# Performance work log

Hardware: AMD Instinct MI355X
Metric: run time of the kernel (lower is better)

## Reference

```python
import jax, jax.numpy as jnp
import numpy as np

V, E, P, T = 65536, 4096, 4096, 512
SENT = 1e9    # finite sentinel for masked min/max (keeps grads NaN-free)
BIG = 1e30    # 'never the minimum' sentinel for invalid points


def setup_inputs() -> dict:
    key = jax.random.key(0)
    k1, k2, k3, k4 = jax.random.split(key, 4)
    verts = jax.random.uniform(k1, (V, 3), dtype=jnp.float32)
    e0 = jax.random.randint(k2, (E,), 0, V - 1)
    edges = jnp.stack([e0, e0 + 1], axis=1)          # distinct endpoints
    listAll = jax.random.randint(k3, (P,), 0, V)
    TableR = jax.random.uniform(k4, (T, 7), dtype=jnp.float32)
    return {"verts": verts, "TableR": TableR, "edges": edges,
            "listAll": listAll, "epoch": 1, "pth": 0}


def _mouth_loss(verts, TableR, edges, listAll):
    v2 = verts[:, :2]                 # deleteaxeZ
    p = v2[listAll]                   # [P,2] query points
    px, py = p[:, 0], p[:, 1]
    ev = v2[edges]                    # [E,2,2]
    x0, y0 = ev[:, 0, 0], ev[:, 0, 1]
    x1, y1 = ev[:, 1, 0], ev[:, 1, 1]
    a = (y0 - y1) / (x0 - x1)         # edge line y = a*x + b (order-invariant)
    b = y0 - a * x0

    # getexpose: first edge with min_x < px < max_x (falls back to last edge)
    xmn, xmx = jnp.minimum(x0, x1), jnp.maximum(x0, x1)
    condA = (px[:, None] > xmn[None, :]) & (px[:, None] < xmx[None, :])  # [P,E]
    idx = jnp.where(condA.any(1), jnp.argmax(condA, axis=1), E - 1)
    exposeY = a[idx] * px + b[idx]
    L1 = jnp.sqrt((py - exposeY) ** 2)        # expose shares x with p -> dx=0
    cy = (py + exposeY) * 0.5                 # centre1 = midpoint (cx == px)
    cx = px

    # getpoints: intersections of horizontal ray y=cy with every edge
    ymn, ymx = jnp.minimum(y0, y1), jnp.maximum(y0, y1)
    condB = (cy[:, None] > ymn[None, :]) & (cy[:, None] < ymx[None, :])  # [P,E]
    xi = (cy[:, None] - b[None, :]) / a[None, :]                          # [P,E]
    n = condB.sum(1)
    xall_mx = jnp.max(jnp.where(condB, xi, -SENT), axis=1)
    xall_mn = jnp.min(jnp.where(condB, xi, SENT), axis=1)
    spu = condB & (xi >= cx[:, None])   # right side (incl. equal, per original)
    inf_ = condB & (xi < cx[:, None])   # left side
    xs = jnp.min(jnp.where(spu, xi, SENT), axis=1)    # minimum of spu
    xinf = jnp.max(jnp.where(inf_, xi, -SENT), axis=1)  # maximum of inf
    has_both = spu.any(1) & inf_.any(1)
    valid = (n == 2) | ((n > 2) & has_both)
    dx = jnp.where(n == 2, xall_mx - xall_mn, xs - xinf)
    L2 = jnp.sqrt(dx ** 2)                    # both points share y=cy
    d1 = jnp.sqrt((cy - 1.0) ** 2)            # dist([1, cy], Ref=(1,1))
    d2 = jnp.sqrt((px - 1.0) ** 2)            # dist([px, 1], Ref=(1,1))

    # al vs every table row (only columns 3..6 are used by the original)
    al = (jnp.abs(L1[:, None] - TableR[None, :, 3])
          + jnp.abs(L2[:, None] - TableR[None, :, 4])
          + jnp.abs(d1[:, None] - TableR[None, :, 5])
          + jnp.abs(d2[:, None] - TableR[None, :, 6]))          # [P,T]
    pm = jnp.min(al, axis=1)                  # per-point best table match
    # `error` is never reset in the original -> running min across points
    m = jnp.where(valid, pm, BIG)
    run = jax.lax.cummin(m, axis=0)
    return jnp.sum(jnp.where(valid, run, 0.0))


def reference(verts, TableR, edges, listAll, epoch, pth):
    # epoch/pth only gate .obj file dumping in the original; no math effect.
    return _mouth_loss(verts, TableR, edges, listAll)
```

## Files before the change

### kernel.cpp

```cpp
#include <hip/hip_runtime.h>
#include <math.h>

#define NV 65536
#define NE 4096
#define NP 4096
#define NT 512
#define SENTF 1000000000.0f
#define BIGF 1e30f

__device__ __forceinline__ float waveMinF(float v) {
    #pragma unroll
    for (int o = 32; o; o >>= 1) v = fminf(v, __shfl_xor(v, o, 64));
    return v;
}
__device__ __forceinline__ float waveMaxF(float v) {
    #pragma unroll
    for (int o = 32; o; o >>= 1) v = fmaxf(v, __shfl_xor(v, o, 64));
    return v;
}
__device__ __forceinline__ int waveSumI(int v) {
    #pragma unroll
    for (int o = 32; o; o >>= 1) v += __shfl_xor(v, o, 64);
    return v;
}
__device__ __forceinline__ int waveMinI(int v) {
    #pragma unroll
    for (int o = 32; o; o >>= 1) v = min(v, __shfl_xor(v, o, 64));
    return v;
}

__global__ void prep_kernel(const float* __restrict__ verts,
                            const int*   __restrict__ edges,
                            const float* __restrict__ tab,
                            float*  __restrict__ ea,  float*  __restrict__ eb,
                            float2* __restrict__ pk2, float4* __restrict__ pk4,
                            float4* __restrict__ tb4) {
    int e = blockIdx.x * blockDim.x + threadIdx.x;
    if (e < NT) {
        const float* r = tab + 7 * e;
        tb4[e] = make_float4(r[3], r[4], r[5], r[6]);
    }
    if (e >= NE) return;
    int i0 = edges[2 * e + 0];
    int i1 = edges[2 * e + 1];
    float x0 = verts[3 * i0 + 0], y0 = verts[3 * i0 + 1];
    float x1 = verts[3 * i1 + 0], y1 = verts[3 * i1 + 1];
    float a = (y0 - y1) / (x0 - x1);
    float b = y0 - a * x0;
    ea[e] = a; eb[e] = b;
    pk2[e] = make_float2(fminf(x0, x1), fmaxf(x0, x1));
    pk4[e] = make_float4(fminf(y0, y1), fmaxf(y0, y1), 1.0f / a, b);
}

__global__ __launch_bounds__(256) void point_kernel(
        const float*  __restrict__ verts,
        const int*    __restrict__ listAll,
        const float*  __restrict__ ea,  const float*  __restrict__ eb,
        const float2* __restrict__ pk2, const float4* __restrict__ pk4,
        const float4* __restrict__ tb4,
        float* __restrict__ mOut, int* __restrict__ validOut) {
    __shared__ int   sIdx[2][2];
    __shared__ float sMx[2][2], sMn[2][2], sXs[2][2], sXi[2][2];
    __shared__ int   sPk[2][2];
    __shared__ float sPm[2][2];

    int tid  = threadIdx.x;
    int lane = tid & 63;
    int wid  = tid >> 6;
    int pr   = wid >> 1;
    int half = wid & 1;
    int p    = blockIdx.x * 2 + pr;

    int   vi = listAll[p];
    float px = verts[3 * vi + 0];
    float py = verts[3 * vi + 1];

    const int base = half * (NE / 2);

    int minIdx = NE;
    for (int it = 0; it < (NE / 2) / 64; ++it) {
        int e = base + it * 64 + lane;
        float2 q = pk2[e];
        bool hit = (px > q.x) && (px < q.y);
        if (hit) minIdx = e;
        if (__any(hit)) break;
    }
    minIdx = waveMinI(minIdx);
    if (lane == 0) sIdx[pr][half] = minIdx;
    __syncthreads();
    int idx = min(sIdx[pr][0], sIdx[pr][1]);
    if (idx >= NE) idx = NE - 1;

    float exposeY = ea[idx] * px + eb[idx];
    float L1 = fabsf(py - exposeY);
    float cy = 0.5f * (py + exposeY);
    float cx = px;

    int   n = 0, hasS = 0, hasI = 0;
    float xallmx = -SENTF, xallmn = SENTF;
    float xs = SENTF, xinf = -SENTF;
    #pragma unroll 8
    for (int e = base + lane; e < base + (NE / 2); e += 64) {
        float4 q = pk4[e];
        bool  c  = (cy > q.x) && (cy < q.y);
        float xi = (cy - q.w) * q.z;
        n += c ? 1 : 0;
        xallmx = fmaxf(xallmx, c ? xi : -SENTF);
        xallmn = fminf(xallmn, c ? xi :  SENTF);
        bool sp = c && (xi >= cx);
        bool in_ = c && (xi <  cx);
        xs   = fminf(xs,   sp  ? xi :  SENTF);
        xinf = fmaxf(xinf, in_ ? xi : -SENTF);
        hasS |= sp ? 1 : 0;
        hasI |= in_ ? 1 : 0;
    }
    int packed = n | (hasS << 16) | (hasI << 24);
    packed = waveSumI(packed);
    xallmx = waveMaxF(xallmx);
    xallmn = waveMinF(xallmn);
    xs     = waveMinF(xs);
    xinf   = waveMaxF(xinf);
    if (lane == 0) {
        sPk[pr][half] = packed;
        sMx[pr][half] = xallmx; sMn[pr][half] = xallmn;
        sXs[pr][half] = xs;     sXi[pr][half] = xinf;
    }
    __syncthreads();
    {
        int pkA = sPk[pr][0], pkB = sPk[pr][1];
        n    = (pkA & 0xFFFF) + (pkB & 0xFFFF);
        hasS = ((pkA >> 16) & 0xFF) + ((pkB >> 16) & 0xFF);
        hasI = ((pkA >> 24) & 0xFF) + ((pkB >> 24) & 0xFF);
        xallmx = fmaxf(sMx[pr][0], sMx[pr][1]);
        xallmn = fminf(sMn[pr][0], sMn[pr][1]);
        xs     = fminf(sXs[pr][0], sXs[pr][1]);
        xinf   = fmaxf(sXi[pr][0], sXi[pr][1]);
    }

    bool valid = (n == 2) || ((n > 2) && (hasS > 0) && (hasI > 0));
    float dx = (n == 2) ? (xallmx - xallmn) : (xs - xinf);
    float L2 = fabsf(dx);
    float d1 = fabsf(cy - 1.0f);
    float d2 = fabsf(px - 1.0f);

    float pm = INFINITY;
    #pragma unroll
    for (int k = 0; k < 4; k++) {
        int t = half * (NT / 2) + k * 64 + lane;
        float4 r = tb4[t];
        float al = fabsf(L1 - r.x) + fabsf(L2 - r.y) +
                   fabsf(d1 - r.z) + fabsf(d2 - r.w);
        pm = fminf(pm, al);
    }
    pm = waveMinF(pm);
    if (lane == 0) sPm[pr][half] = pm;
    __syncthreads();

    if (half == 0 && lane == 0) {
        float pmin = fminf(sPm[pr][0], sPm[pr][1]);
        mOut[p]     = valid ? pmin : BIGF;
        validOut[p] = valid ? 1 : 0;
    }
}

__global__ __launch_bounds__(1024) void scan_kernel(const float* __restrict__ m,
                                                    const int*   __restrict__ valid,
                                                    float* __restrict__ out) {
    __shared__ float wAgg[16];
    __shared__ float wSum[16];
    int t = threadIdx.x;
    int lane = t & 63, wid = t >> 6;

    float v[4]; int vl[4];
    #pragma unroll
    for (int j = 0; j < 4; j++) { v[j] = m[4 * t + j]; vl[j] = valid[4 * t + j]; }
    float cmin = fminf(fminf(v[0], v[1]), fminf(v[2], v[3]));

    float inc = cmin;
    #pragma unroll
    for (int o = 1; o < 64; o <<= 1) {
        float u = __shfl_up(inc, o, 64);
        if (lane >= o) inc = fminf(inc, u);
    }
    if (lane == 63) wAgg[wid] = inc;
    __syncthreads();

    float wavePrefix = INFINITY;
    for (int i = 0; i < wid; i++) wavePrefix = fminf(wavePrefix, wAgg[i]);
    float excl = __shfl_up(inc, 1, 64);
    if (lane == 0) excl = INFINITY;
    float run = fminf(wavePrefix, excl);

    float sum = 0.0f;
    #pragma unroll
    for (int j = 0; j < 4; j++) {
        run = fminf(run, v[j]);
        if (vl[j]) sum += run;
    }
    #pragma unroll
    for (int o = 32; o; o >>= 1) sum += __shfl_xor(sum, o, 64);
    if (lane == 0) wSum[wid] = sum;
    __syncthreads();
    if (t == 0) {
        float s = 0.0f;
        for (int i = 0; i < 16; i++) s += wSum[i];
        out[0] = s;
    }
}

extern "C" void kernel_launch(void* const* d_in, const int* in_sizes, int n_in,
                              void* d_out, int out_size, void* d_ws, size_t ws_size,
                              hipStream_t stream) {
    const float* verts   = (const float*)d_in[0];
    const float* tab     = (const float*)d_in[1];
    const int*   edges   = (const int*)d_in[2];
    const int*   listAll = (const int*)d_in[3];

    char* ws = (char*)d_ws;
    float4* pk4 = (float4*)ws;                     ws += NE * sizeof(float4);
    float4* tb4 = (float4*)ws;                     ws += NT * sizeof(float4);
    float2* pk2 = (float2*)ws;                     ws += NE * sizeof(float2);
    float*  ea  = (float*)ws;                      ws += NE * sizeof(float);
    float*  eb  = (float*)ws;                      ws += NE * sizeof(float);
    float*  mArr= (float*)ws;                      ws += NP * sizeof(float);
    int*    vArr= (int*)ws;

    prep_kernel<<<(NE + 255) / 256, 256, 0, stream>>>(verts, edges, tab, ea, eb, pk2, pk4, tb4);
    point_kernel<<<NP / 2, 256, 0, stream>>>(verts, listAll, ea, eb, pk2, pk4, tb4, mArr, vArr);
    scan_kernel<<<1, 1024, 0, stream>>>(mArr, vArr, (float*)d_out);
}
```

Baseline: 27.42 us.

## Stage edge data in shared memory and assign one wave per point

Point blocks now have 1024 threads and handle 16 points, one wave each. Each block loads the whole packed edge array (64 KB) into LDS once, and every wave reuses it for the ray-intersection scan, which removes repeated global/L2 loads of the same data. Cross-wave shared-memory reductions and most barriers are dropped because each wave covers all edges and table rows for its point. In exchange the block uses 64 KB of LDS, which limits occupancy, and each wave runs a scan twice as long.

Result: slower. 28.94 us (+5.6%).

```diff
diff --git a/kernel.cpp b/kernel.cpp
--- a/kernel.cpp
+++ b/kernel.cpp
@@ -52,62 +52,63 @@
     pk4[e] = make_float4(fminf(y0, y1), fmaxf(y0, y1), 1.0f / a, b);
 }
 
-__global__ __launch_bounds__(256) void point_kernel(
+__global__ __launch_bounds__(1024) void point_kernel(
         const float*  __restrict__ verts,
         const int*    __restrict__ listAll,
         const float*  __restrict__ ea,  const float*  __restrict__ eb,
         const float2* __restrict__ pk2, const float4* __restrict__ pk4,
         const float4* __restrict__ tb4,
         float* __restrict__ mOut, int* __restrict__ validOut) {
-    __shared__ int   sIdx[2][2];
-    __shared__ float sMx[2][2], sMn[2][2], sXs[2][2], sXi[2][2];
-    __shared__ int   sPk[2][2];
-    __shared__ float sPm[2][2];
+    __shared__ float4 sE[NE];
 
     int tid  = threadIdx.x;
     int lane = tid & 63;
     int wid  = tid >> 6;
-    int pr   = wid >> 1;
-    int half = wid & 1;
-    int p    = blockIdx.x * 2 + pr;
+    int p    = blockIdx.x * 16 + wid;
+
+    float4 r0 = pk4[tid];
+    float4 r1 = pk4[1024 + tid];
+    float4 r2 = pk4[2048 + tid];
+    float4 r3 = pk4[3072 + tid];
 
     int   vi = listAll[p];
     float px = verts[3 * vi + 0];
     float py = verts[3 * vi + 1];
 
-    const int base = half * (NE / 2);
-
     int minIdx = NE;
-    for (int it = 0; it < (NE / 2) / 64; ++it) {
-        int e = base + it * 64 + lane;
+    for (int it = 0; it < NE / 64; ++it) {
+        int e = it * 64 + lane;
         float2 q = pk2[e];
         bool hit = (px > q.x) && (px < q.y);
         if (hit) minIdx = e;
         if (__any(hit)) break;
     }
     minIdx = waveMinI(minIdx);
-    if (lane == 0) sIdx[pr][half] = minIdx;
-    __syncthreads();
-    int idx = min(sIdx[pr][0], sIdx[pr][1]);
-    if (idx >= NE) idx = NE - 1;
+    int idx = (minIdx >= NE) ? (NE - 1) : minIdx;
 
     float exposeY = ea[idx] * px + eb[idx];
     float L1 = fabsf(py - exposeY);
     float cy = 0.5f * (py + exposeY);
     float cx = px;
 
+    sE[tid]        = r0;
+    sE[1024 + tid] = r1;
+    sE[2048 + tid] = r2;
+    sE[3072 + tid] = r3;
+    __syncthreads();
+
     int   n = 0, hasS = 0, hasI = 0;
     float xallmx = -SENTF, xallmn = SENTF;
     float xs = SENTF, xinf = -SENTF;
     #pragma unroll 8
-    for (int e = base + lane; e < base + (NE / 2); e += 64) {
-        float4 q = pk4[e];
+    for (int it = 0; it < NE / 64; ++it) {
+        float4 q = sE[it * 64 + lane];
         bool  c  = (cy > q.x) && (cy < q.y);
         float xi = (cy - q.w) * q.z;
         n += c ? 1 : 0;
         xallmx = fmaxf(xallmx, c ? xi : -SENTF);
         xallmn = fminf(xallmn, c ? xi :  SENTF);
-        bool sp = c && (xi >= cx);
+        bool sp  = c && (xi >= cx);
         bool in_ = c && (xi <  cx);
         xs   = fminf(xs,   sp  ? xi :  SENTF);
         xinf = fmaxf(xinf, in_ ? xi : -SENTF);
@@ -120,22 +121,9 @@
     xallmn = waveMinF(xallmn);
     xs     = waveMinF(xs);
     xinf   = waveMaxF(xinf);
-    if (lane == 0) {
-        sPk[pr][half] = packed;
-        sMx[pr][half] = xallmx; sMn[pr][half] = xallmn;
-        sXs[pr][half] = xs;     sXi[pr][half] = xinf;
-    }
-    __syncthreads();
-    {
-        int pkA = sPk[pr][0], pkB = sPk[pr][1];
-        n    = (pkA & 0xFFFF) + (pkB & 0xFFFF);
-        hasS = ((pkA >> 16) & 0xFF) + ((pkB >> 16) & 0xFF);
-        hasI = ((pkA >> 24) & 0xFF) + ((pkB >> 24) & 0xFF);
-        xallmx = fmaxf(sMx[pr][0], sMx[pr][1]);
-        xallmn = fminf(sMn[pr][0], sMn[pr][1]);
-        xs     = fminf(sXs[pr][0], sXs[pr][1]);
-        xinf   = fmaxf(sXi[pr][0], sXi[pr][1]);
-    }
+    n    = packed & 0xFFFF;
+    hasS = (packed >> 16) & 0xFF;
+    hasI = (packed >> 24) & 0xFF;
 
     bool valid = (n == 2) || ((n > 2) && (hasS > 0) && (hasI > 0));
     float dx = (n == 2) ? (xallmx - xallmn) : (xs - xinf);
@@ -145,20 +133,16 @@
 
     float pm = INFINITY;
     #pragma unroll
-    for (int k = 0; k < 4; k++) {
-        int t = half * (NT / 2) + k * 64 + lane;
-        float4 r = tb4[t];
+    for (int k = 0; k < NT / 64; ++k) {
+        float4 r = tb4[k * 64 + lane];
         float al = fabsf(L1 - r.x) + fabsf(L2 - r.y) +
                    fabsf(d1 - r.z) + fabsf(d2 - r.w);
         pm = fminf(pm, al);
     }
     pm = waveMinF(pm);
-    if (lane == 0) sPm[pr][half] = pm;
-    __syncthreads();
-
-    if (half == 0 && lane == 0) {
-        float pmin = fminf(sPm[pr][0], sPm[pr][1]);
-        mOut[p]     = valid ? pmin : BIGF;
+
+    if (lane == 0) {
+        mOut[p]     = valid ? pm : BIGF;
         validOut[p] = valid ? 1 : 0;
     }
 }
@@ -226,6 +210,6 @@
     int*    vArr= (int*)ws;
 
     prep_kernel<<<(NE + 255) / 256, 256, 0, stream>>>(verts, edges, tab, ea, eb, pk2, pk4, tb4);
-    point_kernel<<<NP / 2, 256, 0, stream>>>(verts, listAll, ea, eb, pk2, pk4, tb4, mArr, vArr);
+    point_kernel<<<NP / 16, 1024, 0, stream>>>(verts, listAll, ea, eb, pk2, pk4, tb4, mArr, vArr);
     scan_kernel<<<1, 1024, 0, stream>>>(mArr, vArr, (float*)d_out);
 }
```
